# Kernel tuning notes

Measured on AMD Instinct MI355X. Metric: run time of the kernel, lower is better.

## Reference

```python
import jax, jax.numpy as jnp
import numpy as np

B, N, C = 8, 16384, 4
NUM_GROUPS = 512   # K for farthest point sampling
GROUP_SIZE = 32    # K after energy-based top-k
UPSCALE_K = 512    # ball-query candidate count
RADIUS = 0.5       # group_radius
CONTEXT = 256      # context_length


def _fps_idx(xyz, lengths, K):
    """Iterative farthest point sampling. xyz: (B,P,3). Returns (B,K) int32 indices.
    Start point is index 0 (random_start_point=False). Assumes lengths >= K."""
    Bn, P, _ = xyz.shape
    valid = jnp.arange(P)[None, :] < lengths[:, None]
    start = jnp.zeros((Bn,), jnp.int32)
    mind0 = jnp.full((Bn, P), jnp.float32(1e10))

    def step(carry, _):
        mind, last = carry
        lastpt = jnp.take_along_axis(xyz, last[:, None, None], axis=1)  # (B,1,3)
        d = jnp.sum((xyz - lastpt) ** 2, axis=-1)                       # (B,P)
        mind = jnp.minimum(mind, d)
        nxt = jnp.argmax(jnp.where(valid, mind, -jnp.inf), axis=1).astype(jnp.int32)
        return (mind, nxt), nxt

    _, rest = jax.lax.scan(step, (mind0, start), None, length=K - 1)  # (K-1,B)
    return jnp.concatenate([start[:, None], rest.T], axis=1)          # (B,K)


def _masked_gather(points, idx):
    """torch masked_gather: -1 indices are replaced with 0 before gathering."""
    idx0 = jnp.maximum(idx, 0)
    if idx.ndim == 3:
        Bn, G, K = idx.shape
        out = jnp.take_along_axis(points, idx0.reshape(Bn, G * K)[:, :, None], axis=1)
        return out.reshape(Bn, G, K, points.shape[-1])
    return jnp.take_along_axis(points, idx0[:, :, None], axis=1)


def _ball_query(centers, xyz, lengths, K, radius):
    """First-K points within radius of each center, in original index order; pad -1."""
    P = xyz.shape[1]
    d2 = jnp.sum((centers[:, :, None, :] - xyz[:, None, :, :]) ** 2, axis=-1)  # (B,G,P)
    valid = (d2 < radius * radius) & (jnp.arange(P)[None, None, :] < lengths[:, None, None])
    # key = -index for valid points, -P for invalid -> top_k gives first valid indices
    key = jnp.where(valid, -jnp.arange(P, dtype=jnp.int32)[None, None, :], jnp.int32(-P))
    vals, pos = jax.lax.top_k(key, K)           # (B,G,K)
    return jnp.where(vals > -P, pos, -1)


def _topk_by_energy(points, idx, K):
    """Keep the K highest-energy (channel 3) points per group; pad -1."""
    Bn, G, Ko = idx.shape
    e = points[..., 3]                                                  # (B,P)
    eb = jnp.broadcast_to(e[:, None, :], (Bn, G, e.shape[1]))
    energies = jnp.take_along_axis(eb, jnp.maximum(idx, 0), axis=2)     # (B,G,Ko)
    energies = jnp.where(idx == -1, -jnp.inf, energies)
    top_e, top_pos = jax.lax.top_k(energies, K)
    top_idx = jnp.take_along_axis(idx, top_pos, axis=2)
    return jnp.where(jnp.isneginf(top_e), -1, top_idx)


def setup_inputs() -> dict:
    key = jax.random.key(0)
    k1, k2 = jax.random.split(key)
    points = jax.random.normal(k1, (B, N, C), dtype=jnp.float32)
    lengths = jax.random.randint(k2, (B,), 3 * N // 4, N + 1, dtype=jnp.int32)
    return {"points": points, "lengths": lengths}


def reference(points, lengths):
    # FPS -> group centers (kept with all C channels, as in masked_gather(points, idx))
    centers_idx = _fps_idx(points[:, :, :3], lengths, NUM_GROUPS)
    group_centers = _masked_gather(points, centers_idx)                 # (B,G,C)
    # Ball query around centers
    idx = _ball_query(group_centers[:, :, :3], points[:, :, :3], lengths, UPSCALE_K, RADIUS)
    # Energy-based reduction to GROUP_SIZE points per group
    idx = _topk_by_energy(points, idx, GROUP_SIZE)                      # (B,G,Ks)
    point_lengths = jnp.sum(idx != -1, axis=2)                          # (B,G)
    # fill_empty_indices: replace -1 with the group's first index
    filled = jnp.where(idx == -1, idx[:, :, :1], idx)
    groups = _masked_gather(points, filled)                             # (B,G,Ks,C)
    point_mask = jnp.arange(GROUP_SIZE)[None, None, :] < point_lengths[:, :CONTEXT, None]
    G = idx.shape[1]
    group_lengths = jnp.sum(jnp.all(idx != -1, axis=2), axis=1)         # (B,)
    embedding_mask = jnp.arange(G)[None, :] < group_lengths[:, None]
    return (groups[:, :CONTEXT], group_centers[:, :CONTEXT],
            embedding_mask[:, :CONTEXT], point_mask)
```

## Files before the change

kernel.cpp:

```cpp
#include <hip/hip_runtime.h>
#include <stdint.h>

#define NB   8
#define NP   16384
#define NG   512
#define GS   32
#define UPK  512
#define CTX  256

#define OFF_CENTERS (NB*CTX*GS*4)
#define OFF_EMB     (OFF_CENTERS + NB*CTX*4)
#define OFF_PMASK   (OFF_EMB + NB*CTX)

typedef unsigned long long u64;
typedef unsigned int u32;

__device__ __forceinline__ u32 fkey(float f) {
  union { float f; u32 u; } v; v.f = f;
  u32 s = v.u;
  return s ^ ((s & 0x80000000u) ? 0xFFFFFFFFu : 0x80000000u);
}

__device__ __forceinline__ float dist2(float ax, float ay, float az,
                                       float bx, float by, float bz) {
  float dx = __fsub_rn(ax, bx);
  float dy = __fsub_rn(ay, by);
  float dz = __fsub_rn(az, bz);
  return __fadd_rn(__fadd_rn(__fmul_rn(dx, dx), __fmul_rn(dy, dy)),
                   __fmul_rn(dz, dz));
}

template<int CTRL, int RM>
__device__ __forceinline__ u64 dpp_max_u64(u64 k) {
  int lo = (int)(u32)k, hi = (int)(u32)(k >> 32);
  int mlo = __builtin_amdgcn_update_dpp(lo, lo, CTRL, RM, 0xf, false);
  int mhi = __builtin_amdgcn_update_dpp(hi, hi, CTRL, RM, 0xf, false);
  u64 o = ((u64)(u32)mhi << 32) | (u32)mlo;
  return o > k ? o : k;
}

__device__ __forceinline__ u64 wave_max_u64(u64 k) {
  k = dpp_max_u64<0x111, 0xf>(k);
  k = dpp_max_u64<0x112, 0xf>(k);
  k = dpp_max_u64<0x114, 0xf>(k);
  k = dpp_max_u64<0x118, 0xf>(k);
  k = dpp_max_u64<0x142, 0xa>(k);
  k = dpp_max_u64<0x143, 0xc>(k);
  return k;
}

__device__ __forceinline__ u64 read_lane_u64(u64 k, int lane) {
  u32 lo = (u32)__builtin_amdgcn_readlane((int)(u32)k, lane);
  u32 hi = (u32)__builtin_amdgcn_readlane((int)(u32)(k >> 32), lane);
  return ((u64)hi << 32) | lo;
}

#define FPS_T 512
#define PPT   (NP / FPS_T)

__global__ __launch_bounds__(FPS_T)
__attribute__((amdgpu_waves_per_eu(2, 2)))
void fps_kernel(const float4* __restrict__ pts, const int* __restrict__ lengths,
                float4* __restrict__ centers_ws, int* __restrict__ group_len,
                float* __restrict__ out)
{
  const int b    = blockIdx.x;
  const int tid  = threadIdx.x;
  const int lane = tid & 63;
  const int wave = tid >> 6;
  const float4* p = pts + (size_t)b * NP;
  const int len = lengths[b];
  if (tid == 0) group_len[b] = 0;

  const float4 q0 = p[0];
  float px[PPT], py[PPT], pz[PPT], mind[PPT];
#pragma unroll
  for (int j = 0; j < PPT; j++) {
    int i = tid + j * FPS_T;
    float4 q = p[i];
    if (i >= len) q = q0;
    px[j] = q.x; py[j] = q.y; pz[j] = q.z;
    mind[j] = 1e10f;
  }

  __shared__ u64 sred[2][8];
  __shared__ int s_centers[NG];
  if (tid == 0) s_centers[0] = 0;

  int last = 0;
  for (int it = 1; it < NG; it++) {
    float4 lp = p[last];
    float tmax = -1.0f; int tj = 0;
#pragma unroll
    for (int j = 0; j < PPT; j++) {
      float d = dist2(px[j], py[j], pz[j], lp.x, lp.y, lp.z);
      float m = fminf(mind[j], d);
      mind[j] = m;
      bool c = m > tmax;
      tmax = c ? m : tmax;
      tj   = c ? j : tj;
    }
    int gidx = tid + (tj << 9);
    u64 key = ((u64)__float_as_uint(tmax) << 32) | (u32)(~gidx);
    key = wave_max_u64(key);
    u64 wkey = read_lane_u64(key, 63);
    if (lane == 0) sred[it & 1][wave] = wkey;
    __syncthreads();
    u64 k2 = sred[it & 1][lane & 7];
    k2 = dpp_max_u64<0x111, 0xf>(k2);
    k2 = dpp_max_u64<0x112, 0xf>(k2);
    k2 = dpp_max_u64<0x114, 0xf>(k2);
    u64 bk = read_lane_u64(k2, 7);
    last = (int)(~(u32)bk) & (NP - 1);
    if (tid == 0) s_centers[it] = last;
  }
  __syncthreads();

  {
    int ci = s_centers[tid] & (NP - 1);
    float4 q = p[ci];
    centers_ws[b * NG + tid] = q;
    if (tid < CTX) {
      ((float4*)(out + OFF_CENTERS))[b * CTX + tid] = q;
    }
  }
}

#define BQ_T 256

__global__ __launch_bounds__(BQ_T)
void group_kernel(const float4* __restrict__ pts, const int* __restrict__ lengths,
                  const float4* __restrict__ centers_ws, int* __restrict__ group_len,
                  float* __restrict__ out)
{
  const int blk  = blockIdx.x;
  const int b    = blk & (NB - 1);
  const int g    = blk >> 3;
  const int tid  = threadIdx.x;
  const int lane = tid & 63;
  const int wave = tid >> 6;
  const float4* p = pts + (size_t)b * NP;
  const int len = lengths[b];
  const float4 cc = centers_ws[b * NG + g];

  __shared__ u64 masks[256];
  __shared__ u32 scnt[256];
  __shared__ u32 spre[256];
  __shared__ u32 swsum[4];
  __shared__ float candE[UPK];
  __shared__ int   candI[UPK];
  __shared__ int   s_T, s_pl;
  __shared__ int   s_win[GS];

  if (g >= CTX) {
    u32 c = 0;
    for (int step = 0; step < 64; step++) {
      int i = step * 256 + tid;
      if (i < len) {
        float4 q = p[i];
        float d = dist2(cc.x, cc.y, cc.z, q.x, q.y, q.z);
        c += (d < 0.25f) ? 1u : 0u;
      }
    }
#pragma unroll
    for (int off = 32; off; off >>= 1) c += __shfl_down(c, (unsigned)off, 64);
    if (lane == 0) swsum[wave] = c;
    __syncthreads();
    if (tid == 0) {
      u32 total = swsum[0] + swsum[1] + swsum[2] + swsum[3];
      if (total >= GS) atomicAdd(&group_len[b], 1);
    }
    return;
  }

  for (int step = 0; step < 64; step++) {
    int i = step * 256 + tid;
    bool flag = false;
    if (i < len) {
      float4 q = p[i];
      float d = dist2(cc.x, cc.y, cc.z, q.x, q.y, q.z);
      flag = d < 0.25f;
    }
    u64 m = __ballot(flag);
    if (lane == 0) masks[step * 4 + wave] = m;
  }
  __syncthreads();

  u32 cnt = (u32)__popcll(masks[tid]);
  u32 s = cnt;
#pragma unroll
  for (int off = 1; off < 64; off <<= 1) {
    u32 o = __shfl_up(s, (unsigned)off, 64);
    if (lane >= off) s += o;
  }
  if (lane == 63) swsum[wave] = s;
  __syncthreads();
  u32 woff = 0;
#pragma unroll
  for (int w = 0; w < 4; w++) woff += (w < wave) ? swsum[w] : 0u;
  const u32 total = swsum[0] + swsum[1] + swsum[2] + swsum[3];
  const u32 incl = s + woff;
  scnt[tid] = cnt;
  spre[tid] = incl;

  if (total > UPK) {
    u32 ex = incl - cnt;
    if (ex <= (UPK - 1) && incl > (UPK - 1)) {
      u32 r = (UPK - 1) - ex;
      u64 m = masks[tid];
      for (u32 k = 0; k < r; k++) m &= m - 1;
      s_T = tid * 64 + ((int)__ffsll((unsigned long long)m) - 1);
    }
  } else if (tid == 0) {
    s_T = NP - 1;
  }
  __syncthreads();
  const int T = s_T;

  for (int step = 0; step < 64; step++) {
    int i  = step * 256 + tid;
    int ch = step * 4 + wave;
    u64 m = masks[ch];
    if (((m >> lane) & 1ull) && i <= T) {
      u32 pos = ((spre[ch] - scnt[ch]) +
                 (u32)__popcll(m & ((1ull << lane) - 1ull))) & (UPK - 1);
      candE[pos] = ((const float*)p)[i * 4 + 3];
      candI[pos] = i;
    }
  }
  __syncthreads();

  const int ncand = (int)(total < UPK ? total : UPK);

  if (wave == 0) {
    u64 k[8];
#pragma unroll
    for (int t = 0; t < 8; t++) {
      int ci = lane + t * 64;
      k[t] = (ci < ncand) ? (((u64)fkey(candE[ci]) << 32) | (u32)(~ci)) : 0ull;
    }
    int pl = 0;
    for (int r = 0; r < GS; r++) {
      u64 bm = k[0];
#pragma unroll
      for (int t = 1; t < 8; t++) if (k[t] > bm) bm = k[t];
#pragma unroll
      for (int off = 32; off; off >>= 1) {
        u64 o = __shfl_xor(bm, (unsigned)off, 64);
        if (o > bm) bm = o;
      }
      if (bm == 0) break;
      int pos = (int)(~(u32)bm) & (UPK - 1);
      if (lane == 0) s_win[r] = candI[pos];
      int ol = pos & 63, ot = pos >> 6;
#pragma unroll
      for (int t = 0; t < 8; t++)
        if (t == ot && lane == ol) k[t] = 0;
      pl = r + 1;
    }
    if (lane == 0) {
      int f0 = (pl > 0) ? s_win[0] : 0;
      for (int r = pl; r < GS; r++) s_win[r] = f0;
      s_pl = pl;
    }
  }
  __syncthreads();

  const int base = b * CTX + g;
  if (tid < GS) {
    int fi = s_win[tid] & (NP - 1);
    float4 q = p[fi];
    ((float4*)out)[base * GS + tid] = q;
    out[OFF_PMASK + base * GS + tid] = (tid < s_pl) ? 1.0f : 0.0f;
  }
  if (tid == 0 && total >= GS) atomicAdd(&group_len[b], 1);
}

__global__ void emb_kernel(const int* __restrict__ group_len,
                           float* __restrict__ out)
{
  int i = blockIdx.x * blockDim.x + threadIdx.x;
  if (i < NB * CTX) {
    int b = i >> 8;
    int g = i & 255;
    out[OFF_EMB + i] = (g < group_len[b]) ? 1.0f : 0.0f;
  }
}

extern "C" void kernel_launch(void* const* d_in, const int* in_sizes, int n_in,
                              void* d_out, int out_size, void* d_ws, size_t ws_size,
                              hipStream_t stream)
{
  const float4* pts     = (const float4*)d_in[0];
  const int*    lengths = (const int*)d_in[1];
  float* out = (float*)d_out;

  float4* centers_ws = (float4*)d_ws;
  int*    group_len  = (int*)((char*)d_ws + (size_t)NB * NG * sizeof(float4));

  fps_kernel<<<NB, FPS_T, 0, stream>>>(pts, lengths, centers_ws, group_len, out);
  group_kernel<<<NB * NG, BQ_T, 0, stream>>>(pts, lengths, centers_ws, group_len, out);
  emb_kernel<<<(NB * CTX + 255) / 256, 256, 0, stream>>>(group_len, out);
}
```

Before: 734.0 us.

## Fuse FPS and grouping into persistent kernel with streamed center publication

```diff
diff --git a/kernel.cpp b/kernel.cpp
--- a/kernel.cpp
+++ b/kernel.cpp
@@ -14,6 +14,10 @@
 
 typedef unsigned long long u64;
 typedef unsigned int u32;
+
+#define SENT 0xFFFFFFFFFFFFFFFFull
+#define PUB  32
+#define NWK  31
 
 __device__ __forceinline__ u32 fkey(float f) {
   union { float f; u32 u; } v; v.f = f;
@@ -55,225 +59,269 @@
   return ((u64)hi << 32) | lo;
 }
 
+struct FpsSmem {
+  u64 sred[2][8];
+  int s_centers[NG];
+};
+struct WkSmem {
+  u64 masks[256];
+  u32 scnt[256];
+  u32 spre[256];
+  u32 swsum[8];
+  float candE[UPK];
+  int   candI[UPK];
+  int   s_T, s_pl;
+  int   s_win[GS];
+  u64   s_cc[2];
+};
+union SmemU { FpsSmem f; WkSmem w; };
+struct Smem { SmemU u; char pad[81920]; };
+
+__device__ __forceinline__ void publish_center(u64* __restrict__ cb,
+                                               float* __restrict__ out,
+                                               int b, int w, float4 q) {
+  u64 lo = ((u64)__float_as_uint(q.y) << 32) | __float_as_uint(q.x);
+  u64 hi = ((u64)__float_as_uint(q.w) << 32) | __float_as_uint(q.z);
+  __hip_atomic_store(&cb[2 * w],     lo, __ATOMIC_RELAXED, __HIP_MEMORY_SCOPE_AGENT);
+  __hip_atomic_store(&cb[2 * w + 1], hi, __ATOMIC_RELAXED, __HIP_MEMORY_SCOPE_AGENT);
+  if (w < CTX) ((float4*)(out + OFF_CENTERS))[b * CTX + w] = q;
+}
+
 #define FPS_T 512
 #define PPT   (NP / FPS_T)
 
 __global__ __launch_bounds__(FPS_T)
 __attribute__((amdgpu_waves_per_eu(2, 2)))
-void fps_kernel(const float4* __restrict__ pts, const int* __restrict__ lengths,
-                float4* __restrict__ centers_ws, int* __restrict__ group_len,
-                float* __restrict__ out)
+void fused_kernel(const float4* __restrict__ pts, const int* __restrict__ lengths,
+                  u64* __restrict__ cws, int* __restrict__ group_len,
+                  float* __restrict__ out)
 {
-  const int b    = blockIdx.x;
+  __shared__ Smem sm;
+  const int blk  = blockIdx.x;
   const int tid  = threadIdx.x;
   const int lane = tid & 63;
   const int wave = tid >> 6;
+
+  if (blk < NB) {
+    FpsSmem& F = sm.u.f;
+    const int b = blk;
+    const float4* p = pts + (size_t)b * NP;
+    const int len = lengths[b];
+    u64* cb = cws + (size_t)b * NG * 2;
+
+    const float4 q0 = p[0];
+    float px[PPT], py[PPT], pz[PPT], mind[PPT];
+#pragma unroll
+    for (int j = 0; j < PPT; j++) {
+      int i = tid + j * FPS_T;
+      float4 q = p[i];
+      if (i >= len) q = q0;
+      px[j] = q.x; py[j] = q.y; pz[j] = q.z;
+      mind[j] = 1e10f;
+    }
+    if (tid == 0) F.s_centers[0] = 0;
+
+    int last = 0;
+    for (int it = 1; it < NG; it++) {
+      float4 lp = p[last];
+      float tmax = -1.0f; int tj = 0;
+#pragma unroll
+      for (int j = 0; j < PPT; j++) {
+        float d = dist2(px[j], py[j], pz[j], lp.x, lp.y, lp.z);
+        float m = fminf(mind[j], d);
+        mind[j] = m;
+        bool c = m > tmax;
+        tmax = c ? m : tmax;
+        tj   = c ? j : tj;
+      }
+      int gidx = tid + (tj << 9);
+      u64 key = ((u64)__float_as_uint(tmax) << 32) | (u32)(~gidx);
+      key = wave_max_u64(key);
+      u64 wkey = read_lane_u64(key, 63);
+      if (lane == 0) F.sred[it & 1][wave] = wkey;
+      __syncthreads();
+      u64 k2 = F.sred[it & 1][lane & 7];
+      k2 = dpp_max_u64<0x111, 0xf>(k2);
+      k2 = dpp_max_u64<0x112, 0xf>(k2);
+      k2 = dpp_max_u64<0x114, 0xf>(k2);
+      u64 bk = read_lane_u64(k2, 7);
+      last = (int)(~(u32)bk) & (NP - 1);
+      if (tid == 0) F.s_centers[it] = last;
+      if ((it & (PUB - 1)) == 0 && tid < PUB) {
+        int w = it - PUB + tid;
+        int ci = F.s_centers[w] & (NP - 1);
+        publish_center(cb, out, b, w, p[ci]);
+      }
+    }
+    __syncthreads();
+    if (tid < PUB) {
+      int w = NG - PUB + tid;
+      int ci = F.s_centers[w] & (NP - 1);
+      publish_center(cb, out, b, w, p[ci]);
+    }
+    return;
+  }
+
+  WkSmem& S = sm.u.w;
+  const int b  = blk & (NB - 1);
+  const int wi = (blk >> 3) - 1;
   const float4* p = pts + (size_t)b * NP;
   const int len = lengths[b];
-  if (tid == 0) group_len[b] = 0;
-
-  const float4 q0 = p[0];
-  float px[PPT], py[PPT], pz[PPT], mind[PPT];
-#pragma unroll
-  for (int j = 0; j < PPT; j++) {
-    int i = tid + j * FPS_T;
-    float4 q = p[i];
-    if (i >= len) q = q0;
-    px[j] = q.x; py[j] = q.y; pz[j] = q.z;
-    mind[j] = 1e10f;
-  }
-
-  __shared__ u64 sred[2][8];
-  __shared__ int s_centers[NG];
-  if (tid == 0) s_centers[0] = 0;
-
-  int last = 0;
-  for (int it = 1; it < NG; it++) {
-    float4 lp = p[last];
-    float tmax = -1.0f; int tj = 0;
-#pragma unroll
-    for (int j = 0; j < PPT; j++) {
-      float d = dist2(px[j], py[j], pz[j], lp.x, lp.y, lp.z);
-      float m = fminf(mind[j], d);
-      mind[j] = m;
-      bool c = m > tmax;
-      tmax = c ? m : tmax;
-      tj   = c ? j : tj;
-    }
-    int gidx = tid + (tj << 9);
-    u64 key = ((u64)__float_as_uint(tmax) << 32) | (u32)(~gidx);
-    key = wave_max_u64(key);
-    u64 wkey = read_lane_u64(key, 63);
-    if (lane == 0) sred[it & 1][wave] = wkey;
-    __syncthreads();
-    u64 k2 = sred[it & 1][lane & 7];
-    k2 = dpp_max_u64<0x111, 0xf>(k2);
-    k2 = dpp_max_u64<0x112, 0xf>(k2);
-    k2 = dpp_max_u64<0x114, 0xf>(k2);
-    u64 bk = read_lane_u64(k2, 7);
-    last = (int)(~(u32)bk) & (NP - 1);
-    if (tid == 0) s_centers[it] = last;
-  }
-  __syncthreads();
-
-  {
-    int ci = s_centers[tid] & (NP - 1);
-    float4 q = p[ci];
-    centers_ws[b * NG + tid] = q;
-    if (tid < CTX) {
-      ((float4*)(out + OFF_CENTERS))[b * CTX + tid] = q;
-    }
-  }
-}
-
-#define BQ_T 256
-
-__global__ __launch_bounds__(BQ_T)
-void group_kernel(const float4* __restrict__ pts, const int* __restrict__ lengths,
-                  const float4* __restrict__ centers_ws, int* __restrict__ group_len,
-                  float* __restrict__ out)
-{
-  const int blk  = blockIdx.x;
-  const int b    = blk & (NB - 1);
-  const int g    = blk >> 3;
-  const int tid  = threadIdx.x;
-  const int lane = tid & 63;
-  const int wave = tid >> 6;
-  const float4* p = pts + (size_t)b * NP;
-  const int len = lengths[b];
-  const float4 cc = centers_ws[b * NG + g];
-
-  __shared__ u64 masks[256];
-  __shared__ u32 scnt[256];
-  __shared__ u32 spre[256];
-  __shared__ u32 swsum[4];
-  __shared__ float candE[UPK];
-  __shared__ int   candI[UPK];
-  __shared__ int   s_T, s_pl;
-  __shared__ int   s_win[GS];
-
-  if (g >= CTX) {
-    u32 c = 0;
-    for (int step = 0; step < 64; step++) {
-      int i = step * 256 + tid;
+  u64* cb = cws + (size_t)b * NG * 2;
+
+  for (int g = wi; g < NG; g += NWK) {
+    if (tid == 0) {
+      u64 lo, hi;
+      while ((lo = __hip_atomic_load(&cb[2 * g], __ATOMIC_RELAXED,
+                                     __HIP_MEMORY_SCOPE_AGENT)) == SENT)
+        __builtin_amdgcn_s_sleep(8);
+      while ((hi = __hip_atomic_load(&cb[2 * g + 1], __ATOMIC_RELAXED,
+                                     __HIP_MEMORY_SCOPE_AGENT)) == SENT)
+        __builtin_amdgcn_s_sleep(1);
+      S.s_cc[0] = lo; S.s_cc[1] = hi;
+    }
+    __syncthreads();
+    const float cx = __uint_as_float((u32)S.s_cc[0]);
+    const float cy = __uint_as_float((u32)(S.s_cc[0] >> 32));
+    const float cz = __uint_as_float((u32)S.s_cc[1]);
+
+    if (g >= CTX) {
+      u32 c = 0;
+      for (int step = 0; step < 32; step++) {
+        int i = step * 512 + tid;
+        if (i < len) {
+          float4 q = p[i];
+          float d = dist2(cx, cy, cz, q.x, q.y, q.z);
+          c += (d < 0.25f) ? 1u : 0u;
+        }
+      }
+#pragma unroll
+      for (int off = 32; off; off >>= 1) c += __shfl_down(c, (unsigned)off, 64);
+      if (lane == 0) S.swsum[wave] = c;
+      __syncthreads();
+      if (tid == 0) {
+        u32 total = 0;
+#pragma unroll
+        for (int w = 0; w < 8; w++) total += S.swsum[w];
+        if (total >= GS) atomicAdd(&group_len[b], 1);
+      }
+      __syncthreads();
+      continue;
+    }
+
+    for (int step = 0; step < 32; step++) {
+      int i = step * 512 + tid;
+      bool flag = false;
       if (i < len) {
         float4 q = p[i];
-        float d = dist2(cc.x, cc.y, cc.z, q.x, q.y, q.z);
-        c += (d < 0.25f) ? 1u : 0u;
-      }
-    }
-#pragma unroll
-    for (int off = 32; off; off >>= 1) c += __shfl_down(c, (unsigned)off, 64);
-    if (lane == 0) swsum[wave] = c;
-    __syncthreads();
-    if (tid == 0) {
-      u32 total = swsum[0] + swsum[1] + swsum[2] + swsum[3];
-      if (total >= GS) atomicAdd(&group_len[b], 1);
-    }
-    return;
+        float d = dist2(cx, cy, cz, q.x, q.y, q.z);
+        flag = d < 0.25f;
+      }
+      u64 m = __ballot(flag);
+      if (lane == 0) S.masks[step * 8 + wave] = m;
+    }
+    __syncthreads();
+
+    u32 cnt = 0, sc = 0;
+    if (tid < 256) {
+      cnt = (u32)__popcll(S.masks[tid]);
+      sc = cnt;
+#pragma unroll
+      for (int off = 1; off < 64; off <<= 1) {
+        u32 o = __shfl_up(sc, (unsigned)off, 64);
+        if (lane >= off) sc += o;
+      }
+      if (lane == 63) S.swsum[wave] = sc;
+    }
+    __syncthreads();
+    const u32 total = S.swsum[0] + S.swsum[1] + S.swsum[2] + S.swsum[3];
+    if (tid < 256) {
+      u32 woff = 0;
+#pragma unroll
+      for (int w = 0; w < 4; w++) woff += (w < wave) ? S.swsum[w] : 0u;
+      u32 incl = sc + woff;
+      S.scnt[tid] = cnt;
+      S.spre[tid] = incl;
+      if (total > UPK) {
+        u32 ex = incl - cnt;
+        if (ex <= (UPK - 1) && incl > (UPK - 1)) {
+          u32 r = (UPK - 1) - ex;
+          u64 m = S.masks[tid];
+          for (u32 k = 0; k < r; k++) m &= m - 1;
+          S.s_T = tid * 64 + ((int)__ffsll((unsigned long long)m) - 1);
+        }
+      } else if (tid == 0) S.s_T = NP - 1;
+    }
+    __syncthreads();
+    const int T = S.s_T;
+
+    for (int step = 0; step < 32; step++) {
+      int i  = step * 512 + tid;
+      int ch = step * 8 + wave;
+      u64 m = S.masks[ch];
+      if (((m >> lane) & 1ull) && i <= T) {
+        u32 pos = ((S.spre[ch] - S.scnt[ch]) +
+                   (u32)__popcll(m & ((1ull << lane) - 1ull))) & (UPK - 1);
+        S.candE[pos] = ((const float*)p)[i * 4 + 3];
+        S.candI[pos] = i;
+      }
+    }
+    __syncthreads();
+
+    const int ncand = (int)(total < UPK ? total : UPK);
+
+    if (wave == 0) {
+      u64 k[8];
+#pragma unroll
+      for (int t = 0; t < 8; t++) {
+        int ci = lane + t * 64;
+        k[t] = (ci < ncand) ? (((u64)fkey(S.candE[ci]) << 32) | (u32)(~ci)) : 0ull;
+      }
+      int pl = 0;
+      for (int r = 0; r < GS; r++) {
+        u64 bm = k[0];
+#pragma unroll
+        for (int t = 1; t < 8; t++) if (k[t] > bm) bm = k[t];
+#pragma unroll
+        for (int off = 32; off; off >>= 1) {
+          u64 o = __shfl_xor(bm, (unsigned)off, 64);
+          if (o > bm) bm = o;
+        }
+        if (bm == 0) break;
+        int pos = (int)(~(u32)bm) & (UPK - 1);
+        if (lane == 0) S.s_win[r] = S.candI[pos];
+        int ol = pos & 63, ot = pos >> 6;
+#pragma unroll
+        for (int t = 0; t < 8; t++)
+          if (t == ot && lane == ol) k[t] = 0;
+        pl = r + 1;
+      }
+      if (lane == 0) {
+        int f0 = (pl > 0) ? S.s_win[0] : 0;
+        for (int r = pl; r < GS; r++) S.s_win[r] = f0;
+        S.s_pl = pl;
+      }
+    }
+    __syncthreads();
+
+    const int base = b * CTX + g;
+    if (tid < GS) {
+      int fi = S.s_win[tid] & (NP - 1);
+      float4 q = p[fi];
+      ((float4*)out)[base * GS + tid] = q;
+      out[OFF_PMASK + base * GS + tid] = (tid < S.s_pl) ? 1.0f : 0.0f;
+    }
+    if (tid == 0 && total >= GS) atomicAdd(&group_len[b], 1);
+    __syncthreads();
   }
-
-  for (int step = 0; step < 64; step++) {
-    int i = step * 256 + tid;
-    bool flag = false;
-    if (i < len) {
-      float4 q = p[i];
-      float d = dist2(cc.x, cc.y, cc.z, q.x, q.y, q.z);
-      flag = d < 0.25f;
-    }
-    u64 m = __ballot(flag);
-    if (lane == 0) masks[step * 4 + wave] = m;
-  }
-  __syncthreads();
-
-  u32 cnt = (u32)__popcll(masks[tid]);
-  u32 s = cnt;
-#pragma unroll
-  for (int off = 1; off < 64; off <<= 1) {
-    u32 o = __shfl_up(s, (unsigned)off, 64);
-    if (lane >= off) s += o;
-  }
-  if (lane == 63) swsum[wave] = s;
-  __syncthreads();
-  u32 woff = 0;
-#pragma unroll
-  for (int w = 0; w < 4; w++) woff += (w < wave) ? swsum[w] : 0u;
-  const u32 total = swsum[0] + swsum[1] + swsum[2] + swsum[3];
-  const u32 incl = s + woff;
-  scnt[tid] = cnt;
-  spre[tid] = incl;
-
-  if (total > UPK) {
-    u32 ex = incl - cnt;
-    if (ex <= (UPK - 1) && incl > (UPK - 1)) {
-      u32 r = (UPK - 1) - ex;
-      u64 m = masks[tid];
-      for (u32 k = 0; k < r; k++) m &= m - 1;
-      s_T = tid * 64 + ((int)__ffsll((unsigned long long)m) - 1);
-    }
-  } else if (tid == 0) {
-    s_T = NP - 1;
-  }
-  __syncthreads();
-  const int T = s_T;
-
-  for (int step = 0; step < 64; step++) {
-    int i  = step * 256 + tid;
-    int ch = step * 4 + wave;
-    u64 m = masks[ch];
-    if (((m >> lane) & 1ull) && i <= T) {
-      u32 pos = ((spre[ch] - scnt[ch]) +
-                 (u32)__popcll(m & ((1ull << lane) - 1ull))) & (UPK - 1);
-      candE[pos] = ((const float*)p)[i * 4 + 3];
-      candI[pos] = i;
-    }
-  }
-  __syncthreads();
-
-  const int ncand = (int)(total < UPK ? total : UPK);
-
-  if (wave == 0) {
-    u64 k[8];
-#pragma unroll
-    for (int t = 0; t < 8; t++) {
-      int ci = lane + t * 64;
-      k[t] = (ci < ncand) ? (((u64)fkey(candE[ci]) << 32) | (u32)(~ci)) : 0ull;
-    }
-    int pl = 0;
-    for (int r = 0; r < GS; r++) {
-      u64 bm = k[0];
-#pragma unroll
-      for (int t = 1; t < 8; t++) if (k[t] > bm) bm = k[t];
-#pragma unroll
-      for (int off = 32; off; off >>= 1) {
-        u64 o = __shfl_xor(bm, (unsigned)off, 64);
-        if (o > bm) bm = o;
-      }
-      if (bm == 0) break;
-      int pos = (int)(~(u32)bm) & (UPK - 1);
-      if (lane == 0) s_win[r] = candI[pos];
-      int ol = pos & 63, ot = pos >> 6;
-#pragma unroll
-      for (int t = 0; t < 8; t++)
-        if (t == ot && lane == ol) k[t] = 0;
-      pl = r + 1;
-    }
-    if (lane == 0) {
-      int f0 = (pl > 0) ? s_win[0] : 0;
-      for (int r = pl; r < GS; r++) s_win[r] = f0;
-      s_pl = pl;
-    }
-  }
-  __syncthreads();
-
-  const int base = b * CTX + g;
-  if (tid < GS) {
-    int fi = s_win[tid] & (NP - 1);
-    float4 q = p[fi];
-    ((float4*)out)[base * GS + tid] = q;
-    out[OFF_PMASK + base * GS + tid] = (tid < s_pl) ? 1.0f : 0.0f;
-  }
-  if (tid == 0 && total >= GS) atomicAdd(&group_len[b], 1);
+}
+
+__global__ void init_kernel(u64* __restrict__ cws, int* __restrict__ group_len)
+{
+  int i = blockIdx.x * blockDim.x + threadIdx.x;
+  if (i < NB * NG * 2)
+    __hip_atomic_store(&cws[i], SENT, __ATOMIC_RELAXED, __HIP_MEMORY_SCOPE_AGENT);
+  if (i < NB) group_len[i] = 0;
 }
 
 __global__ void emb_kernel(const int* __restrict__ group_len,
@@ -295,10 +343,10 @@
   const int*    lengths = (const int*)d_in[1];
   float* out = (float*)d_out;
 
-  float4* centers_ws = (float4*)d_ws;
-  int*    group_len  = (int*)((char*)d_ws + (size_t)NB * NG * sizeof(float4));
-
-  fps_kernel<<<NB, FPS_T, 0, stream>>>(pts, lengths, centers_ws, group_len, out);
-  group_kernel<<<NB * NG, BQ_T, 0, stream>>>(pts, lengths, centers_ws, group_len, out);
+  u64* cws       = (u64*)d_ws;
+  int* group_len = (int*)((char*)d_ws + (size_t)NB * NG * sizeof(float4));
+
+  init_kernel<<<(NB * NG * 2 + 255) / 256, 256, 0, stream>>>(cws, group_len);
+  fused_kernel<<<NB + NB * NWK, FPS_T, 0, stream>>>(pts, lengths, cws, group_len, out);
   emb_kernel<<<(NB * CTX + 255) / 256, 256, 0, stream>>>(group_len, out);
 }
```

Measured after the change: 707.1 us. 3.7% less time.
